# Kernel tuning notes

Hardware: AMD Instinct MI355X
Metric: run time of the kernel (lower is better)

The kernel has to match this reference:

```python
import jax, jax.numpy as jnp
import numpy as np

MEMORY_SLOTS = 256
MEMORY_TOPK = 8
RETRIEVAL_WEIGHT = 0.5


def setup_inputs() -> dict:
    key = jax.random.key(0)
    ks = jax.random.split(key, 5)
    B, T, C = 8, 2048, 1024
    scale = 1.0 / np.sqrt(C)
    return {
        "x": jax.random.normal(ks[0], (B, T, C), dtype=jnp.float32),
        "Wq": jax.random.normal(ks[1], (C, C), dtype=jnp.float32) * scale,
        "Wk": jax.random.normal(ks[2], (C, C), dtype=jnp.float32) * scale,
        "Wv": jax.random.normal(ks[3], (C, C), dtype=jnp.float32) * scale,
        "Wp": jax.random.normal(ks[4], (C, C), dtype=jnp.float32) * scale,
    }


def reference(x, Wq, Wk, Wv, Wp):
    B, T, C = x.shape
    num_slots = min(T, MEMORY_SLOTS)
    topk = min(num_slots, MEMORY_TOPK)
    # adaptive_avg_pool1d with T divisible by num_slots == mean over equal chunks
    slots = x.reshape(B, num_slots, T // num_slots, C).mean(axis=2)  # [B,S,C]
    # Linear layers (torch: x @ W.T, no bias)
    q = jnp.einsum("btc,dc->btd", x, Wq)        # [B,T,C]
    k = jnp.einsum("bsc,dc->bsd", slots, Wk)    # [B,S,C]
    v = jnp.einsum("bsc,dc->bsd", slots, Wv)    # [B,S,C]
    scores = jnp.einsum("btd,bsd->bts", q, k) * (1.0 / jnp.sqrt(jnp.float32(C)))
    topk_scores, topk_indices = jax.lax.top_k(scores, topk)  # [B,T,K]
    topk_weights = jax.nn.softmax(topk_scores, axis=-1)       # [B,T,K]
    # gather selected value rows: [B,T,K,C]
    retrieved = jnp.take_along_axis(v[:, None, :, :], topk_indices[..., None], axis=2)
    retrieved = jnp.einsum("btkc,btk->btc", retrieved, topk_weights)
    out = jnp.einsum("btc,dc->btd", retrieved, Wp) * RETRIEVAL_WEIGHT
    return out
```

## Files before the change

kernel.cpp:

```cpp
#include <hip/hip_runtime.h>
#include <cstdint>
#include <cstddef>

#define Tt 2048
#define Cc 1024
#define Ss 256

using short8 = __attribute__((ext_vector_type(8))) short;
using f32x4  = __attribute__((ext_vector_type(4))) float;
typedef const __attribute__((address_space(1))) void* as1_cvp;
typedef __attribute__((address_space(3))) void* as3_vp;

__device__ __forceinline__ unsigned short f2bf(float f) {
  unsigned int u = __float_as_uint(f);
  u += 0x7fffu + ((u >> 16) & 1u);
  return (unsigned short)(u >> 16);
}
__device__ __forceinline__ float bf2f(unsigned short h) {
  return __uint_as_float(((unsigned)h) << 16);
}
__device__ __forceinline__ void split3(float v, unsigned short& h, unsigned short& m, unsigned short& l) {
  h = f2bf(v);
  float r = v - bf2f(h);
  m = f2bf(r);
  l = f2bf(r - bf2f(m));
}

__device__ __forceinline__ int sw32(int row, int q) {
  return row * 32 + ((q ^ ((row >> 1) & 3)) << 3);
}

__global__ __launch_bounds__(256) void poolsplit_k(const float* __restrict__ x, unsigned short* __restrict__ sp) {
  const long PS2 = 2048l * 1024;
  const int sli = blockIdx.x;
  const int c = threadIdx.x << 2;
  const float* src = x + (size_t)sli * 8 * Cc + c;
  float a[4] = {0.f, 0.f, 0.f, 0.f};
#pragma unroll
  for (int j = 0; j < 8; j++) {
    float4 v = *(const float4*)(src + (size_t)j * Cc);
    a[0] += v.x; a[1] += v.y; a[2] += v.z; a[3] += v.w;
  }
  unsigned short h[4], m[4], l[4];
#pragma unroll
  for (int e = 0; e < 4; e++) split3(a[e] * 0.125f, h[e], m[e], l[e]);
  size_t o = (size_t)sli * Cc + c;
  *(uint2*)&sp[o]           = uint2{(unsigned)h[0] | ((unsigned)h[1] << 16), (unsigned)h[2] | ((unsigned)h[3] << 16)};
  *(uint2*)&sp[o + PS2]     = uint2{(unsigned)m[0] | ((unsigned)m[1] << 16), (unsigned)m[2] | ((unsigned)m[3] << 16)};
  *(uint2*)&sp[o + 2 * PS2] = uint2{(unsigned)l[0] | ((unsigned)l[1] << 16), (unsigned)l[2] | ((unsigned)l[3] << 16)};
}

__global__ __launch_bounds__(256) void split_t_k(const float* __restrict__ src, unsigned short* __restrict__ dst,
                                                 long pstride, int npl) {
  __shared__ unsigned short th[64][68], tm[64][68], tl[64][68];
  const int r0 = blockIdx.y << 6, c0 = blockIdx.x << 6;
  const int tid = threadIdx.x;
#pragma unroll
  for (int p = 0; p < 4; p++) {
    int r = (p << 4) + (tid >> 4);
    int c = (tid & 15) << 2;
    float4 v = *(const float4*)&src[(size_t)(r0 + r) * Cc + c0 + c];
    unsigned short h, m, l;
    split3(v.x, h, m, l); th[c + 0][r] = h; tm[c + 0][r] = m; tl[c + 0][r] = l;
    split3(v.y, h, m, l); th[c + 1][r] = h; tm[c + 1][r] = m; tl[c + 1][r] = l;
    split3(v.z, h, m, l); th[c + 2][r] = h; tm[c + 2][r] = m; tl[c + 2][r] = l;
    split3(v.w, h, m, l); th[c + 3][r] = h; tm[c + 3][r] = m; tl[c + 3][r] = l;
  }
  __syncthreads();
#pragma unroll
  for (int p = 0; p < 4; p++) {
    int r = (p << 4) + (tid >> 4);
    int c = (tid & 15) << 2;
    size_t o = (size_t)(c0 + r) * Cc + r0 + c;
    *(uint2*)&dst[o] = uint2{(unsigned)th[r][c] | ((unsigned)th[r][c+1] << 16),
                             (unsigned)th[r][c+2] | ((unsigned)th[r][c+3] << 16)};
    *(uint2*)&dst[o + pstride] = uint2{(unsigned)tm[r][c] | ((unsigned)tm[r][c+1] << 16),
                                       (unsigned)tm[r][c+2] | ((unsigned)tm[r][c+3] << 16)};
    if (npl == 3)
      *(uint2*)&dst[o + 2 * pstride] = uint2{(unsigned)tl[r][c] | ((unsigned)tl[r][c+1] << 16),
                                             (unsigned)tl[r][c+2] | ((unsigned)tl[r][c+3] << 16)};
  }
}

__global__ __launch_bounds__(256) void split_k(const float* __restrict__ src, unsigned short* __restrict__ dst,
                                               long pstride, int npl) {
  int id = blockIdx.x * 256 + threadIdx.x;
  int c = id << 2;
  float4 v = *(const float4*)&src[c];
  unsigned short h[4], m[4], l[4];
  split3(v.x, h[0], m[0], l[0]); split3(v.y, h[1], m[1], l[1]);
  split3(v.z, h[2], m[2], l[2]); split3(v.w, h[3], m[3], l[3]);
  *(uint2*)&dst[c] = uint2{(unsigned)h[0] | ((unsigned)h[1] << 16), (unsigned)h[2] | ((unsigned)h[3] << 16)};
  *(uint2*)&dst[c + pstride] = uint2{(unsigned)m[0] | ((unsigned)m[1] << 16), (unsigned)m[2] | ((unsigned)m[3] << 16)};
  if (npl == 3)
    *(uint2*)&dst[c + 2 * pstride] = uint2{(unsigned)l[0] | ((unsigned)l[1] << 16), (unsigned)l[2] | ((unsigned)l[3] << 16)};
}

template<int NT, int SPLIT_OUT>
__device__ __forceinline__ void gemm3_body(const unsigned short* __restrict__ Ap, long apl,
                                           const unsigned short* __restrict__ Bp, long bpl,
                                           float* __restrict__ C,
                                           unsigned short* __restrict__ Cs, long cpl,
                                           float scale) {
  constexpr int NPL = (NT == 6) ? 3 : 2;
  constexpr int BUFS = 2 * NPL * 2048;
  __shared__ unsigned short LDS[2 * BUFS];
  const int tid = threadIdx.x, lane = tid & 63, wid = tid >> 6;
  const int m0 = blockIdx.y << 6, n0 = blockIdx.x << 6;

  const unsigned short* sp[2 * NPL];
  int dof[2 * NPL];
#pragma unroll
  for (int i = 0; i < 2 * NPL; i++) {
    int s = wid * 2 * NPL + i;
    int tile = s >> 2;
    int ci = ((s & 3) << 6) | lane;
    int row = ci >> 2;
    int q = (ci & 3) ^ ((row >> 1) & 3);
    int isB = tile >= NPL;
    int pl = isB ? tile - NPL : tile;
    const unsigned short* base = isB ? (Bp + (size_t)pl * bpl) : (Ap + (size_t)pl * apl);
    int r0 = isB ? n0 : m0;
    sp[i] = base + (size_t)(r0 + row) * Cc + (q << 3);
    dof[i] = (tile * 2048 + ((s & 3) << 9)) * 2;
  }

  const int wm = (wid >> 1) << 5, wn = (wid & 1) << 5;
  const int lm = lane & 15, lq = lane >> 4;
  constexpr int PA[6] = {0, 0, 1, 0, 2, 1};
  constexpr int PB[6] = {0, 1, 0, 2, 0, 1};
  const f32x4 zero = {0.f, 0.f, 0.f, 0.f};
  f32x4 acc[2][2] = {{zero, zero}, {zero, zero}};

#pragma unroll
  for (int i = 0; i < 2 * NPL; i++) {
    __builtin_amdgcn_global_load_lds((as1_cvp)sp[i], (as3_vp)((char*)LDS + dof[i]), 16, 0, 0);
    sp[i] += 32;
  }
  __syncthreads();

  int cur = 0;
  for (int k0 = 0; k0 < Cc; k0 += 32) {
    if (k0 + 32 < Cc) {
      const int nb = (cur ^ 1) * (BUFS * 2);
#pragma unroll
      for (int i = 0; i < 2 * NPL; i++) {
        __builtin_amdgcn_global_load_lds((as1_cvp)sp[i], (as3_vp)((char*)LDS + nb + dof[i]), 16, 0, 0);
        sp[i] += 32;
      }
    }
    const int cb = cur * BUFS;
    short8 af[2][NPL], bf[2][NPL];
#pragma unroll
    for (int i = 0; i < 2; i++)
#pragma unroll
      for (int p = 0; p < NPL; p++) {
        af[i][p] = *(const short8*)&LDS[cb + p * 2048 + sw32(wm + (i << 4) + lm, lq)];
        bf[i][p] = *(const short8*)&LDS[cb + (NPL + p) * 2048 + sw32(wn + (i << 4) + lm, lq)];
      }
#pragma unroll
    for (int i = 0; i < 2; i++)
#pragma unroll
      for (int j = 0; j < 2; j++)
#pragma unroll
        for (int t = 0; t < NT; t++)
          acc[i][j] = __builtin_amdgcn_mfma_f32_16x16x32_bf16(af[i][PA[t]], bf[j][PB[t]], acc[i][j], 0, 0, 0);
    __syncthreads();
    cur ^= 1;
  }
#pragma unroll
  for (int i = 0; i < 2; i++)
#pragma unroll
    for (int j = 0; j < 2; j++)
#pragma unroll
      for (int r = 0; r < 4; r++) {
        int gr = m0 + wm + (i << 4) + (lq << 2) + r;
        int gc = n0 + wn + (j << 4) + lm;
        size_t o = (size_t)gr * Cc + gc;
        float v = acc[i][j][r] * scale;
        if (SPLIT_OUT) {
          unsigned short h = f2bf(v);
          float rr = v - bf2f(h);
          unsigned short mm2 = f2bf(rr);
          Cs[o] = h;
          Cs[o + cpl] = mm2;
          if (NPL == 3) Cs[o + 2 * (size_t)cpl] = f2bf(rr - bf2f(mm2));
        } else {
          C[o] = v;
        }
      }
}

__global__ __launch_bounds__(256) void gemm3_61_k(const unsigned short* __restrict__ Ap, long apl,
                                                  const unsigned short* __restrict__ Bp, long bpl,
                                                  unsigned short* __restrict__ Cs, long cpl, float scale) {
  gemm3_body<6, 1>(Ap, apl, Bp, bpl, nullptr, Cs, cpl, scale);
}
__global__ __launch_bounds__(256) void gemm3_31_k(const unsigned short* __restrict__ Ap, long apl,
                                                  const unsigned short* __restrict__ Bp, long bpl,
                                                  unsigned short* __restrict__ Cs, long cpl, float scale) {
  gemm3_body<3, 1>(Ap, apl, Bp, bpl, nullptr, Cs, cpl, scale);
}
__global__ __launch_bounds__(256) void gemm3_30_k(const unsigned short* __restrict__ Ap, long apl,
                                                  const unsigned short* __restrict__ Bp, long bpl,
                                                  float* __restrict__ C, float scale) {
  gemm3_body<3, 0>(Ap, apl, Bp, bpl, C, nullptr, 0, scale);
}

__global__ __launch_bounds__(512) void scores_topk_k(const float* __restrict__ x,
                                                     const unsigned short* __restrict__ kqp,
                                                     float* __restrict__ topw, int* __restrict__ topi) {
  __shared__ __align__(16) char smem[125952];
  unsigned short* lds16 = (unsigned short*)smem;
  float* sc = (float*)smem;

  const int tid = threadIdx.x, lane = tid & 63, wid = tid >> 6;
  const int bid = blockIdx.x;
  const int b = bid & 7, tt = bid >> 3;

  const char* ksrc[6];
  int kdst[6];
#pragma unroll
  for (int i = 0; i < 6; i++) {
    int s = wid * 6 + i;
    int p = s >> 4, sub = s & 15;
    int ci = (sub << 6) | lane;
    int row = ci >> 2;
    int q = (ci & 3) ^ ((row >> 1) & 3);
    ksrc[i] = (const char*)(kqp + (size_t)p * (2048l * 1024) + ((size_t)b * Ss + row) * Cc + (q << 3));
    kdst[i] = p * 16384 + sub * 1024;
  }
  const int spr = tid >> 3, spk = (tid & 7) << 2;
  const float* xsrc = x + ((size_t)b * Tt + (size_t)tt * 64 + spr) * Cc + spk;

  const int wm = (wid & 1) << 5;
  const int wn = (wid >> 1) << 6;
  const int lm = lane & 15, lq = lane >> 4;
  const int XP = 49152;

  constexpr int PA[6] = {0, 0, 1, 0, 2, 1};
  constexpr int PB[6] = {0, 1, 0, 2, 0, 1};
  const f32x4 zero = {0.f, 0.f, 0.f, 0.f};
  f32x4 acc[2][4];
#pragma unroll
  for (int i = 0; i < 2; i++)
#pragma unroll
    for (int j = 0; j < 4; j++) acc[i][j] = zero;

  {
    float4 xv = *(const float4*)xsrc; xsrc += 32;
#pragma unroll
    for (int i = 0; i < 6; i++) {
      __builtin_amdgcn_global_load_lds((as1_cvp)ksrc[i], (as3_vp)(smem + kdst[i]), 16, 0, 0);
      ksrc[i] += 64;
    }
    unsigned short h[4], m[4], l[4];
    split3(xv.x, h[0], m[0], l[0]); split3(xv.y, h[1], m[1], l[1]);
    split3(xv.z, h[2], m[2], l[2]); split3(xv.w, h[3], m[3], l[3]);
    int o = XP + spr * 36 + spk;
    *(uint2*)&lds16[o]        = uint2{(unsigned)h[0] | ((unsigned)h[1] << 16), (unsigned)h[2] | ((unsigned)h[3] << 16)};
    *(uint2*)&lds16[o + 2304] = uint2{(unsigned)m[0] | ((unsigned)m[1] << 16), (unsigned)m[2] | ((unsigned)m[3] << 16)};
    *(uint2*)&lds16[o + 4608] = uint2{(unsigned)l[0] | ((unsigned)l[1] << 16), (unsigned)l[2] | ((unsigned)l[3] << 16)};
  }
  __syncthreads();

  int cur = 0;
  for (int ks = 0; ks < 32; ks++) {
    const int nb = cur ^ 1;
    float4 xv2;
    if (ks < 31) {
      xv2 = *(const float4*)xsrc; xsrc += 32;
#pragma unroll
      for (int i = 0; i < 6; i++) {
        __builtin_amdgcn_global_load_lds((as1_cvp)ksrc[i], (as3_vp)(smem + nb * 49152 + kdst[i]), 16, 0, 0);
        ksrc[i] += 64;
      }
    }
    const int xb = XP + cur * 6912;
    const int kb = cur * 24576;
    short8 afr[2][3], bfr[4][3];
#pragma unroll
    for (int i = 0; i < 2; i++)
#pragma unroll
      for (int p = 0; p < 3; p++)
        afr[i][p] = *(const short8*)&lds16[xb + p * 2304 + (wm + (i << 4) + lm) * 36 + (lq << 3)];
#pragma unroll
    for (int j = 0; j < 4; j++) {
      int br = wn + (j << 4) + lm;
      int bo = (br << 5) + ((lq ^ ((br >> 1) & 3)) << 3);
#pragma unroll
      for (int p = 0; p < 3; p++)
        bfr[j][p] = *(const short8*)&lds16[kb + p * 8192 + bo];
    }
#pragma unroll
    for (int i = 0; i < 2; i++)
#pragma unroll
      for (int j = 0; j < 4; j++)
#pragma unroll
        for (int t = 0; t < 6; t++)
          acc[i][j] = __builtin_amdgcn_mfma_f32_16x16x32_bf16(afr[i][PA[t]], bfr[j][PB[t]], acc[i][j], 0, 0, 0);
    if (ks < 31) {
      unsigned short h[4], m[4], l[4];
      split3(xv2.x, h[0], m[0], l[0]); split3(xv2.y, h[1], m[1], l[1]);
      split3(xv2.z, h[2], m[2], l[2]); split3(xv2.w, h[3], m[3], l[3]);
      int o = XP + nb * 6912 + spr * 36 + spk;
      *(uint2*)&lds16[o]        = uint2{(unsigned)h[0] | ((unsigned)h[1] << 16), (unsigned)h[2] | ((unsigned)h[3] << 16)};
      *(uint2*)&lds16[o + 2304] = uint2{(unsigned)m[0] | ((unsigned)m[1] << 16), (unsigned)m[2] | ((unsigned)m[3] << 16)};
      *(uint2*)&lds16[o + 4608] = uint2{(unsigned)l[0] | ((unsigned)l[1] << 16), (unsigned)l[2] | ((unsigned)l[3] << 16)};
    }
    __syncthreads();
    cur ^= 1;
  }

#pragma unroll
  for (int i = 0; i < 2; i++)
#pragma unroll
    for (int j = 0; j < 4; j++)
#pragma unroll
      for (int r = 0; r < 4; r++)
        sc[(wm + (i << 4) + (lq << 2) + r) * 260 + wn + (j << 4) + lm] = acc[i][j][r] * 0.03125f;
  __syncthreads();

  for (int r2 = 0; r2 < 8; r2++) {
    int row = (wid << 3) + r2;
    float4 v = *(const float4*)(sc + row * 260 + (lane << 2));
    float cand[4] = {v.x, v.y, v.z, v.w};
    float topv[8]; int tops[8];
#pragma unroll
    for (int k = 0; k < 8; k++) {
      float bv = -1e30f; int bs = 1 << 20;
#pragma unroll
      for (int e = 0; e < 4; e++) {
        int s = (lane << 2) + e;
        if (cand[e] > bv || (cand[e] == bv && s < bs)) { bv = cand[e]; bs = s; }
      }
#pragma unroll
      for (int m = 32; m >= 1; m >>= 1) {
        float ov = __shfl_xor(bv, m, 64);
        int   os = __shfl_xor(bs, m, 64);
        if (ov > bv || (ov == bv && os < bs)) { bv = ov; bs = os; }
      }
      topv[k] = bv; tops[k] = bs;
      if ((bs >> 2) == lane) cand[bs & 3] = -1e30f;
    }
    float mx = topv[0];
    float sum = 0.f;
#pragma unroll
    for (int k = 0; k < 8; k++) sum += expf(topv[k] - mx);
    if (lane < 8) {
      float myv = topv[0]; int myi = tops[0];
#pragma unroll
      for (int k = 1; k < 8; k++) if (lane == k) { myv = topv[k]; myi = tops[k]; }
      size_t trow = (size_t)b * Tt + (size_t)tt * 64 + row;
      topw[trow * 8 + lane] = expf(myv - mx) / sum;
      topi[trow * 8 + lane] = myi;
    }
  }
}

__global__ __launch_bounds__(256) void gatherout_k(const float* __restrict__ u, const float* __restrict__ topw,
                                                   const int* __restrict__ topi, float* __restrict__ out) {
  __shared__ float w[8];
  __shared__ int  id8[8];
  const int row = blockIdx.x;
  const int b = row >> 11;
  if (threadIdx.x < 8) {
    w[threadIdx.x]   = topw[(size_t)row * 8 + threadIdx.x];
    id8[threadIdx.x] = topi[(size_t)row * 8 + threadIdx.x];
  }
  __syncthreads();
  int c = threadIdx.x << 2;
  float ax = 0.f, ay = 0.f, az = 0.f, aw = 0.f;
#pragma unroll
  for (int j = 0; j < 8; j++) {
    const float4 vv = *(const float4*)&u[((size_t)(b << 8) + id8[j]) * Cc + c];
    float wj = w[j];
    ax = fmaf(wj, vv.x, ax); ay = fmaf(wj, vv.y, ay);
    az = fmaf(wj, vv.z, az); aw = fmaf(wj, vv.w, aw);
  }
  *(float4*)&out[(size_t)row * Cc + c] = make_float4(ax * 0.5f, ay * 0.5f, az * 0.5f, aw * 0.5f);
}

extern "C" void kernel_launch(void* const* d_in, const int* in_sizes, int n_in,
                              void* d_out, int out_size, void* d_ws, size_t ws_size,
                              hipStream_t stream) {
  (void)in_sizes; (void)n_in; (void)out_size; (void)ws_size;
  const float* x  = (const float*)d_in[0];
  const float* Wq = (const float*)d_in[1];
  const float* Wk = (const float*)d_in[2];
  const float* Wv = (const float*)d_in[3];
  const float* Wp = (const float*)d_in[4];
  float* out = (float*)d_out;

  char* ws = (char*)d_ws;
  const size_t MB = 1ull << 20;
  const long PS1 = 1024l * 1024;
  const long PS2 = 2048l * 1024;
  unsigned short* slotp = (unsigned short*)(ws + 0 * MB);
  unsigned short* Wqt   = (unsigned short*)(ws + 12 * MB);
  unsigned short* Wkt   = (unsigned short*)(ws + 18 * MB);
  unsigned short* Wvt   = (unsigned short*)(ws + 24 * MB);
  unsigned short* Wpp   = (unsigned short*)(ws + 28 * MB);
  unsigned short* MtT   = (unsigned short*)(ws + 32 * MB);
  unsigned short* kqp   = (unsigned short*)(ws + 38 * MB);
  unsigned short* W2p   = (unsigned short*)(ws + 50 * MB);
  float*          u     = (float*)(ws + 54 * MB);
  float*          topw  = (float*)(ws + 62 * MB);
  int*            topi  = (int*)(ws + 62 * MB + 512 * 1024);

  poolsplit_k<<<2048, 256, 0, stream>>>(x, slotp);
  split_t_k<<<dim3(16, 16), 256, 0, stream>>>(Wq, Wqt, PS1, 3);
  split_t_k<<<dim3(16, 16), 256, 0, stream>>>(Wk, Wkt, PS1, 3);
  split_t_k<<<dim3(16, 16), 256, 0, stream>>>(Wv, Wvt, PS1, 2);
  split_k<<<1024, 256, 0, stream>>>(Wp, Wpp, PS1, 2);
  gemm3_61_k<<<dim3(16, 16), 256, 0, stream>>>(Wqt, PS1, Wkt, PS1, MtT, PS1, 1.0f);
  gemm3_61_k<<<dim3(16, 32), 256, 0, stream>>>(slotp, PS2, MtT, PS1, kqp, PS2, 1.0f);
  gemm3_31_k<<<dim3(16, 16), 256, 0, stream>>>(Wpp, PS1, Wvt, PS1, W2p, PS1, 1.0f);
  gemm3_30_k<<<dim3(16, 32), 256, 0, stream>>>(slotp, PS2, W2p, PS1, u, 1.0f);
  scores_topk_k<<<256, 512, 0, stream>>>(x, kqp, topw, topi);
  gatherout_k<<<16384, 256, 0, stream>>>(u, topw, topi, out);
}
```

Before: 380.2 us.

## Split scores/top-k over slot halves and merge partial top-8 lists

The scores+top-k kernel now handles only half of the 256 memory slots per block, which doubles the grid from 256 to 512 blocks and halves LDS use and accumulator registers. Each block writes a partial top-8 with global slot indices, and a new topmerge kernel merges the two halves and applies the softmax. The goal is better occupancy on a GPU with many CUs, since 256 blocks under-fill the device. The cost is that every block redoes the x-tile loading and 3-way bf16 splitting, plus an extra launch and a round trip of the partial lists through global memory.

New measurement: 418.6 us. +10.1%, slower.

```diff
diff --git a/kernel.cpp b/kernel.cpp
--- a/kernel.cpp
+++ b/kernel.cpp
@@ -207,57 +207,55 @@
   gemm3_body<3, 0>(Ap, apl, Bp, bpl, C, nullptr, 0, scale);
 }
 
-__global__ __launch_bounds__(512) void scores_topk_k(const float* __restrict__ x,
-                                                     const unsigned short* __restrict__ kqp,
-                                                     float* __restrict__ topw, int* __restrict__ topi) {
-  __shared__ __align__(16) char smem[125952];
+__global__ __launch_bounds__(512, 4) void scores_topk_k(const float* __restrict__ x,
+                                                        const unsigned short* __restrict__ kqp,
+                                                        float* __restrict__ hv, int* __restrict__ hi) {
+  __shared__ __align__(16) char smem[76800];
   unsigned short* lds16 = (unsigned short*)smem;
   float* sc = (float*)smem;
 
   const int tid = threadIdx.x, lane = tid & 63, wid = tid >> 6;
   const int bid = blockIdx.x;
-  const int b = bid & 7, tt = bid >> 3;
-
-  const char* ksrc[6];
-  int kdst[6];
-#pragma unroll
-  for (int i = 0; i < 6; i++) {
-    int s = wid * 6 + i;
-    int p = s >> 4, sub = s & 15;
+  const int b = bid & 7, half = (bid >> 3) & 1, tt = bid >> 4;
+  const int s0 = half << 7;
+
+  const char* ksrc[3];
+  int kdst[3];
+#pragma unroll
+  for (int i = 0; i < 3; i++) {
+    int s = wid * 3 + i;
+    int p = s >> 3, sub = s & 7;
     int ci = (sub << 6) | lane;
     int row = ci >> 2;
     int q = (ci & 3) ^ ((row >> 1) & 3);
-    ksrc[i] = (const char*)(kqp + (size_t)p * (2048l * 1024) + ((size_t)b * Ss + row) * Cc + (q << 3));
-    kdst[i] = p * 16384 + sub * 1024;
+    ksrc[i] = (const char*)(kqp + (size_t)p * (2048l * 1024) + ((size_t)b * Ss + s0 + row) * Cc + (q << 3));
+    kdst[i] = p * 8192 + sub * 1024;
   }
   const int spr = tid >> 3, spk = (tid & 7) << 2;
   const float* xsrc = x + ((size_t)b * Tt + (size_t)tt * 64 + spr) * Cc + spk;
 
   const int wm = (wid & 1) << 5;
-  const int wn = (wid >> 1) << 6;
+  const int wn = (wid >> 1) << 5;
   const int lm = lane & 15, lq = lane >> 4;
-  const int XP = 49152;
+  const int XPs = 24576;
+  const int KQB = 24576;
 
   constexpr int PA[6] = {0, 0, 1, 0, 2, 1};
   constexpr int PB[6] = {0, 1, 0, 2, 0, 1};
   const f32x4 zero = {0.f, 0.f, 0.f, 0.f};
-  f32x4 acc[2][4];
-#pragma unroll
-  for (int i = 0; i < 2; i++)
-#pragma unroll
-    for (int j = 0; j < 4; j++) acc[i][j] = zero;
+  f32x4 acc[2][2] = {{zero, zero}, {zero, zero}};
 
   {
     float4 xv = *(const float4*)xsrc; xsrc += 32;
 #pragma unroll
-    for (int i = 0; i < 6; i++) {
+    for (int i = 0; i < 3; i++) {
       __builtin_amdgcn_global_load_lds((as1_cvp)ksrc[i], (as3_vp)(smem + kdst[i]), 16, 0, 0);
       ksrc[i] += 64;
     }
     unsigned short h[4], m[4], l[4];
     split3(xv.x, h[0], m[0], l[0]); split3(xv.y, h[1], m[1], l[1]);
     split3(xv.z, h[2], m[2], l[2]); split3(xv.w, h[3], m[3], l[3]);
-    int o = XP + spr * 36 + spk;
+    int o = XPs + spr * 36 + spk;
     *(uint2*)&lds16[o]        = uint2{(unsigned)h[0] | ((unsigned)h[1] << 16), (unsigned)h[2] | ((unsigned)h[3] << 16)};
     *(uint2*)&lds16[o + 2304] = uint2{(unsigned)m[0] | ((unsigned)m[1] << 16), (unsigned)m[2] | ((unsigned)m[3] << 16)};
     *(uint2*)&lds16[o + 4608] = uint2{(unsigned)l[0] | ((unsigned)l[1] << 16), (unsigned)l[2] | ((unsigned)l[3] << 16)};
@@ -271,31 +269,31 @@
     if (ks < 31) {
       xv2 = *(const float4*)xsrc; xsrc += 32;
 #pragma unroll
-      for (int i = 0; i < 6; i++) {
-        __builtin_amdgcn_global_load_lds((as1_cvp)ksrc[i], (as3_vp)(smem + nb * 49152 + kdst[i]), 16, 0, 0);
+      for (int i = 0; i < 3; i++) {
+        __builtin_amdgcn_global_load_lds((as1_cvp)ksrc[i], (as3_vp)(smem + nb * KQB + kdst[i]), 16, 0, 0);
         ksrc[i] += 64;
       }
     }
-    const int xb = XP + cur * 6912;
-    const int kb = cur * 24576;
-    short8 afr[2][3], bfr[4][3];
+    const int xb = XPs + cur * 6912;
+    const int kb = cur * 12288;
+    short8 afr[2][3], bfr[2][3];
 #pragma unroll
     for (int i = 0; i < 2; i++)
 #pragma unroll
       for (int p = 0; p < 3; p++)
         afr[i][p] = *(const short8*)&lds16[xb + p * 2304 + (wm + (i << 4) + lm) * 36 + (lq << 3)];
 #pragma unroll
-    for (int j = 0; j < 4; j++) {
+    for (int j = 0; j < 2; j++) {
       int br = wn + (j << 4) + lm;
       int bo = (br << 5) + ((lq ^ ((br >> 1) & 3)) << 3);
 #pragma unroll
       for (int p = 0; p < 3; p++)
-        bfr[j][p] = *(const short8*)&lds16[kb + p * 8192 + bo];
+        bfr[j][p] = *(const short8*)&lds16[kb + p * 4096 + bo];
     }
 #pragma unroll
     for (int i = 0; i < 2; i++)
 #pragma unroll
-      for (int j = 0; j < 4; j++)
+      for (int j = 0; j < 2; j++)
 #pragma unroll
         for (int t = 0; t < 6; t++)
           acc[i][j] = __builtin_amdgcn_mfma_f32_16x16x32_bf16(afr[i][PA[t]], bfr[j][PB[t]], acc[i][j], 0, 0, 0);
@@ -303,7 +301,7 @@
       unsigned short h[4], m[4], l[4];
       split3(xv2.x, h[0], m[0], l[0]); split3(xv2.y, h[1], m[1], l[1]);
       split3(xv2.z, h[2], m[2], l[2]); split3(xv2.w, h[3], m[3], l[3]);
-      int o = XP + nb * 6912 + spr * 36 + spk;
+      int o = XPs + nb * 6912 + spr * 36 + spk;
       *(uint2*)&lds16[o]        = uint2{(unsigned)h[0] | ((unsigned)h[1] << 16), (unsigned)h[2] | ((unsigned)h[3] << 16)};
       *(uint2*)&lds16[o + 2304] = uint2{(unsigned)m[0] | ((unsigned)m[1] << 16), (unsigned)m[2] | ((unsigned)m[3] << 16)};
       *(uint2*)&lds16[o + 4608] = uint2{(unsigned)l[0] | ((unsigned)l[1] << 16), (unsigned)l[2] | ((unsigned)l[3] << 16)};
@@ -315,23 +313,23 @@
 #pragma unroll
   for (int i = 0; i < 2; i++)
 #pragma unroll
-    for (int j = 0; j < 4; j++)
+    for (int j = 0; j < 2; j++)
 #pragma unroll
       for (int r = 0; r < 4; r++)
-        sc[(wm + (i << 4) + (lq << 2) + r) * 260 + wn + (j << 4) + lm] = acc[i][j][r] * 0.03125f;
+        sc[(wm + (i << 4) + (lq << 2) + r) * 132 + wn + (j << 4) + lm] = acc[i][j][r] * 0.03125f;
   __syncthreads();
 
   for (int r2 = 0; r2 < 8; r2++) {
     int row = (wid << 3) + r2;
-    float4 v = *(const float4*)(sc + row * 260 + (lane << 2));
-    float cand[4] = {v.x, v.y, v.z, v.w};
+    float2 v2 = *(const float2*)(sc + row * 132 + (lane << 1));
+    float cand[2] = {v2.x, v2.y};
     float topv[8]; int tops[8];
 #pragma unroll
     for (int k = 0; k < 8; k++) {
       float bv = -1e30f; int bs = 1 << 20;
 #pragma unroll
-      for (int e = 0; e < 4; e++) {
-        int s = (lane << 2) + e;
+      for (int e = 0; e < 2; e++) {
+        int s = (lane << 1) + e;
         if (cand[e] > bv || (cand[e] == bv && s < bs)) { bv = cand[e]; bs = s; }
       }
 #pragma unroll
@@ -341,20 +339,51 @@
         if (ov > bv || (ov == bv && os < bs)) { bv = ov; bs = os; }
       }
       topv[k] = bv; tops[k] = bs;
-      if ((bs >> 2) == lane) cand[bs & 3] = -1e30f;
-    }
-    float mx = topv[0];
-    float sum = 0.f;
-#pragma unroll
-    for (int k = 0; k < 8; k++) sum += expf(topv[k] - mx);
+      if ((bs >> 1) == lane) cand[bs & 1] = -1e30f;
+    }
     if (lane < 8) {
       float myv = topv[0]; int myi = tops[0];
 #pragma unroll
       for (int k = 1; k < 8; k++) if (lane == k) { myv = topv[k]; myi = tops[k]; }
       size_t trow = (size_t)b * Tt + (size_t)tt * 64 + row;
-      topw[trow * 8 + lane] = expf(myv - mx) / sum;
-      topi[trow * 8 + lane] = myi;
-    }
+      hv[trow * 16 + (half << 3) + lane] = myv;
+      hi[trow * 16 + (half << 3) + lane] = s0 + myi;
+    }
+  }
+}
+
+__global__ __launch_bounds__(256) void topmerge_k(const float* __restrict__ hv, const int* __restrict__ hi,
+                                                  float* __restrict__ topw, int* __restrict__ topi) {
+  const int row = blockIdx.x * 256 + threadIdx.x;
+  float v[16]; int ix[16];
+#pragma unroll
+  for (int g = 0; g < 4; g++) {
+    float4 a = *(const float4*)(hv + (size_t)row * 16 + (g << 2));
+    int4  c = *(const int4*)(hi + (size_t)row * 16 + (g << 2));
+    v[(g << 2) + 0] = a.x; v[(g << 2) + 1] = a.y; v[(g << 2) + 2] = a.z; v[(g << 2) + 3] = a.w;
+    ix[(g << 2) + 0] = c.x; ix[(g << 2) + 1] = c.y; ix[(g << 2) + 2] = c.z; ix[(g << 2) + 3] = c.w;
+  }
+  float ov[8]; int oi[8];
+#pragma unroll
+  for (int k = 0; k < 8; k++) {
+    float bv = -1e30f; int bi = 1 << 30;
+#pragma unroll
+    for (int e = 0; e < 16; e++)
+      if (v[e] > bv || (v[e] == bv && ix[e] < bi)) { bv = v[e]; bi = ix[e]; }
+    ov[k] = bv; oi[k] = bi;
+#pragma unroll
+    for (int e = 0; e < 16; e++)
+      if (v[e] == bv && ix[e] == bi) v[e] = -1e30f;
+  }
+  const float mx = ov[0];
+  float w[8]; float sum = 0.f;
+#pragma unroll
+  for (int k = 0; k < 8; k++) { w[k] = expf(ov[k] - mx); sum += w[k]; }
+  const float inv = 1.f / sum;
+#pragma unroll
+  for (int k = 0; k < 8; k++) {
+    topw[(size_t)row * 8 + k] = w[k] * inv;
+    topi[(size_t)row * 8 + k] = oi[k];
   }
 }
 
@@ -407,6 +436,8 @@
   float*          u     = (float*)(ws + 54 * MB);
   float*          topw  = (float*)(ws + 62 * MB);
   int*            topi  = (int*)(ws + 62 * MB + 512 * 1024);
+  float*          hv    = (float*)(ws + 63 * MB);
+  int*            hi    = (int*)(ws + 64 * MB);
 
   poolsplit_k<<<2048, 256, 0, stream>>>(x, slotp);
   split_t_k<<<dim3(16, 16), 256, 0, stream>>>(Wq, Wqt, PS1, 3);
@@ -417,6 +448,7 @@
   gemm3_61_k<<<dim3(16, 32), 256, 0, stream>>>(slotp, PS2, MtT, PS1, kqp, PS2, 1.0f);
   gemm3_31_k<<<dim3(16, 16), 256, 0, stream>>>(Wpp, PS1, Wvt, PS1, W2p, PS1, 1.0f);
   gemm3_30_k<<<dim3(16, 32), 256, 0, stream>>>(slotp, PS2, W2p, PS1, u, 1.0f);
-  scores_topk_k<<<256, 512, 0, stream>>>(x, kqp, topw, topi);
+  scores_topk_k<<<512, 512, 0, stream>>>(x, kqp, hv, hi);
+  topmerge_k<<<64, 256, 0, stream>>>(hv, hi, topw, topi);
   gatherout_k<<<16384, 256, 0, stream>>>(u, topw, topi, out);
 }
```

## Load K fragments directly from global into registers, shrink LDS for two blocks/CU

Applied to the files above, without the earlier changes.

The scores/top-k kernel no longer stages the three-way-split K matrix through double-buffered LDS with global_load_lds. Each wave now reads its B fragments straight from global memory into registers every k-step. Only the x tile stays in LDS. This cuts the shared memory footprint enough to request two 512-thread blocks per CU, aiming for higher occupancy. The trade-off is that the global load latency of K is no longer prefetched, so it sits directly in front of the MFMAs, and there is redundant global traffic across waves that share columns.

New measurement: 404.6 us. +6.4%, slower.

```diff
diff --git a/kernel.cpp b/kernel.cpp
--- a/kernel.cpp
+++ b/kernel.cpp
@@ -207,10 +207,10 @@
   gemm3_body<3, 0>(Ap, apl, Bp, bpl, C, nullptr, 0, scale);
 }
 
-__global__ __launch_bounds__(512) void scores_topk_k(const float* __restrict__ x,
-                                                     const unsigned short* __restrict__ kqp,
-                                                     float* __restrict__ topw, int* __restrict__ topi) {
-  __shared__ __align__(16) char smem[125952];
+__global__ __launch_bounds__(512, 2) void scores_topk_k(const float* __restrict__ x,
+                                                        const unsigned short* __restrict__ kqp,
+                                                        float* __restrict__ topw, int* __restrict__ topi) {
+  __shared__ __align__(16) char smem[66560];
   unsigned short* lds16 = (unsigned short*)smem;
   float* sc = (float*)smem;
 
@@ -218,25 +218,15 @@
   const int bid = blockIdx.x;
   const int b = bid & 7, tt = bid >> 3;
 
-  const char* ksrc[6];
-  int kdst[6];
-#pragma unroll
-  for (int i = 0; i < 6; i++) {
-    int s = wid * 6 + i;
-    int p = s >> 4, sub = s & 15;
-    int ci = (sub << 6) | lane;
-    int row = ci >> 2;
-    int q = (ci & 3) ^ ((row >> 1) & 3);
-    ksrc[i] = (const char*)(kqp + (size_t)p * (2048l * 1024) + ((size_t)b * Ss + row) * Cc + (q << 3));
-    kdst[i] = p * 16384 + sub * 1024;
-  }
   const int spr = tid >> 3, spk = (tid & 7) << 2;
   const float* xsrc = x + ((size_t)b * Tt + (size_t)tt * 64 + spr) * Cc + spk;
 
   const int wm = (wid & 1) << 5;
   const int wn = (wid >> 1) << 6;
   const int lm = lane & 15, lq = lane >> 4;
-  const int XP = 49152;
+
+  const long KPL = 2048l * 1024;
+  const unsigned short* kqb = kqp + ((size_t)b * Ss + wn + lm) * Cc + (lq << 3);
 
   constexpr int PA[6] = {0, 0, 1, 0, 2, 1};
   constexpr int PB[6] = {0, 1, 0, 2, 0, 1};
@@ -249,15 +239,10 @@
 
   {
     float4 xv = *(const float4*)xsrc; xsrc += 32;
-#pragma unroll
-    for (int i = 0; i < 6; i++) {
-      __builtin_amdgcn_global_load_lds((as1_cvp)ksrc[i], (as3_vp)(smem + kdst[i]), 16, 0, 0);
-      ksrc[i] += 64;
-    }
     unsigned short h[4], m[4], l[4];
     split3(xv.x, h[0], m[0], l[0]); split3(xv.y, h[1], m[1], l[1]);
     split3(xv.z, h[2], m[2], l[2]); split3(xv.w, h[3], m[3], l[3]);
-    int o = XP + spr * 36 + spk;
+    int o = spr * 36 + spk;
     *(uint2*)&lds16[o]        = uint2{(unsigned)h[0] | ((unsigned)h[1] << 16), (unsigned)h[2] | ((unsigned)h[3] << 16)};
     *(uint2*)&lds16[o + 2304] = uint2{(unsigned)m[0] | ((unsigned)m[1] << 16), (unsigned)m[2] | ((unsigned)m[3] << 16)};
     *(uint2*)&lds16[o + 4608] = uint2{(unsigned)l[0] | ((unsigned)l[1] << 16), (unsigned)l[2] | ((unsigned)l[3] << 16)};
@@ -267,31 +252,22 @@
   int cur = 0;
   for (int ks = 0; ks < 32; ks++) {
     const int nb = cur ^ 1;
+    const int k0 = ks << 5;
     float4 xv2;
-    if (ks < 31) {
-      xv2 = *(const float4*)xsrc; xsrc += 32;
-#pragma unroll
-      for (int i = 0; i < 6; i++) {
-        __builtin_amdgcn_global_load_lds((as1_cvp)ksrc[i], (as3_vp)(smem + nb * 49152 + kdst[i]), 16, 0, 0);
-        ksrc[i] += 64;
-      }
-    }
-    const int xb = XP + cur * 6912;
-    const int kb = cur * 24576;
-    short8 afr[2][3], bfr[4][3];
+    if (ks < 31) { xv2 = *(const float4*)xsrc; xsrc += 32; }
+    short8 bfr[4][3];
+#pragma unroll
+    for (int j = 0; j < 4; j++)
+#pragma unroll
+      for (int p = 0; p < 3; p++)
+        bfr[j][p] = *(const short8*)(kqb + (size_t)p * KPL + (size_t)(j << 4) * Cc + k0);
+    const int xb = cur * 6912;
+    short8 afr[2][3];
 #pragma unroll
     for (int i = 0; i < 2; i++)
 #pragma unroll
       for (int p = 0; p < 3; p++)
         afr[i][p] = *(const short8*)&lds16[xb + p * 2304 + (wm + (i << 4) + lm) * 36 + (lq << 3)];
-#pragma unroll
-    for (int j = 0; j < 4; j++) {
-      int br = wn + (j << 4) + lm;
-      int bo = (br << 5) + ((lq ^ ((br >> 1) & 3)) << 3);
-#pragma unroll
-      for (int p = 0; p < 3; p++)
-        bfr[j][p] = *(const short8*)&lds16[kb + p * 8192 + bo];
-    }
 #pragma unroll
     for (int i = 0; i < 2; i++)
 #pragma unroll
@@ -303,7 +279,7 @@
       unsigned short h[4], m[4], l[4];
       split3(xv2.x, h[0], m[0], l[0]); split3(xv2.y, h[1], m[1], l[1]);
       split3(xv2.z, h[2], m[2], l[2]); split3(xv2.w, h[3], m[3], l[3]);
-      int o = XP + nb * 6912 + spr * 36 + spk;
+      int o = nb * 6912 + spr * 36 + spk;
       *(uint2*)&lds16[o]        = uint2{(unsigned)h[0] | ((unsigned)h[1] << 16), (unsigned)h[2] | ((unsigned)h[3] << 16)};
       *(uint2*)&lds16[o + 2304] = uint2{(unsigned)m[0] | ((unsigned)m[1] << 16), (unsigned)m[2] | ((unsigned)m[3] << 16)};
       *(uint2*)&lds16[o + 4608] = uint2{(unsigned)l[0] | ((unsigned)l[1] << 16), (unsigned)l[2] | ((unsigned)l[3] << 16)};
```

## Batch independent GEMMs into shared launches and use 128x128 tiles for slot GEMMs

Applied to the files above, without the earlier changes.

Merges the two independent weight-product GEMMs into a single launch that picks its branch from blockIdx.z. It does the same for the two slot GEMMs, and those now use a new 128x128-tile body with 4x4 MFMA accumulators per wave. The aim is to cut launch count, fill more CUs per launch, and raise data reuse per LDS tile in the larger GEMMs. The cost is more LDS (96KB) and more registers per block, which may lower occupancy. The z=0 and z=1 branches also do unequal amounts of work, so the load is imbalanced.

After: 361.9 us. 4.8% less time.

```diff
diff --git a/kernel.cpp b/kernel.cpp
--- a/kernel.cpp
+++ b/kernel.cpp
@@ -97,14 +97,14 @@
 }
 
 template<int NT, int SPLIT_OUT>
-__device__ __forceinline__ void gemm3_body(const unsigned short* __restrict__ Ap, long apl,
+__device__ __forceinline__ void gemm3_body(unsigned short* LDS,
+                                           const unsigned short* __restrict__ Ap, long apl,
                                            const unsigned short* __restrict__ Bp, long bpl,
                                            float* __restrict__ C,
                                            unsigned short* __restrict__ Cs, long cpl,
                                            float scale) {
   constexpr int NPL = (NT == 6) ? 3 : 2;
   constexpr int BUFS = 2 * NPL * 2048;
-  __shared__ unsigned short LDS[2 * BUFS];
   const int tid = threadIdx.x, lane = tid & 63, wid = tid >> 6;
   const int m0 = blockIdx.y << 6, n0 = blockIdx.x << 6;
 
@@ -191,20 +191,131 @@
       }
 }
 
-__global__ __launch_bounds__(256) void gemm3_61_k(const unsigned short* __restrict__ Ap, long apl,
-                                                  const unsigned short* __restrict__ Bp, long bpl,
-                                                  unsigned short* __restrict__ Cs, long cpl, float scale) {
-  gemm3_body<6, 1>(Ap, apl, Bp, bpl, nullptr, Cs, cpl, scale);
-}
-__global__ __launch_bounds__(256) void gemm3_31_k(const unsigned short* __restrict__ Ap, long apl,
-                                                  const unsigned short* __restrict__ Bp, long bpl,
-                                                  unsigned short* __restrict__ Cs, long cpl, float scale) {
-  gemm3_body<3, 1>(Ap, apl, Bp, bpl, nullptr, Cs, cpl, scale);
-}
-__global__ __launch_bounds__(256) void gemm3_30_k(const unsigned short* __restrict__ Ap, long apl,
-                                                  const unsigned short* __restrict__ Bp, long bpl,
-                                                  float* __restrict__ C, float scale) {
-  gemm3_body<3, 0>(Ap, apl, Bp, bpl, C, nullptr, 0, scale);
+template<int NT, int SPLIT_OUT>
+__device__ __forceinline__ void gemm128_body(unsigned short* LDS,
+                                             const unsigned short* __restrict__ Ap, long apl,
+                                             const unsigned short* __restrict__ Bp, long bpl,
+                                             float* __restrict__ C,
+                                             unsigned short* __restrict__ Cs, long cpl,
+                                             float scale) {
+  constexpr int NPL = (NT == 6) ? 3 : 2;
+  constexpr int BUFS = 2 * NPL * 4096;
+  const int tid = threadIdx.x, lane = tid & 63, wid = tid >> 6;
+  const int m0 = blockIdx.y << 7, n0 = blockIdx.x << 7;
+
+  const unsigned short* sp[4 * NPL];
+  int dof[4 * NPL];
+#pragma unroll
+  for (int i = 0; i < 4 * NPL; i++) {
+    int s = wid * 4 * NPL + i;
+    int tile = s >> 3;
+    int ci = ((s & 7) << 6) | lane;
+    int row = ci >> 2;
+    int q = (ci & 3) ^ ((row >> 1) & 3);
+    int isB = tile >= NPL;
+    int pl = isB ? tile - NPL : tile;
+    const unsigned short* base = isB ? (Bp + (size_t)pl * bpl) : (Ap + (size_t)pl * apl);
+    int r0 = isB ? n0 : m0;
+    sp[i] = base + (size_t)(r0 + row) * Cc + (q << 3);
+    dof[i] = (tile * 4096 + ((s & 7) << 9)) * 2;
+  }
+
+  const int wr = (wid >> 1) << 6, wc = (wid & 1) << 6;
+  const int lm = lane & 15, lq = lane >> 4;
+  constexpr int PA[6] = {0, 0, 1, 0, 2, 1};
+  constexpr int PB[6] = {0, 1, 0, 2, 0, 1};
+  const f32x4 zero = {0.f, 0.f, 0.f, 0.f};
+  f32x4 acc[4][4];
+#pragma unroll
+  for (int i = 0; i < 4; i++)
+#pragma unroll
+    for (int j = 0; j < 4; j++) acc[i][j] = zero;
+
+#pragma unroll
+  for (int i = 0; i < 4 * NPL; i++) {
+    __builtin_amdgcn_global_load_lds((as1_cvp)sp[i], (as3_vp)((char*)LDS + dof[i]), 16, 0, 0);
+    sp[i] += 32;
+  }
+  __syncthreads();
+
+  int cur = 0;
+  for (int k0 = 0; k0 < Cc; k0 += 32) {
+    if (k0 + 32 < Cc) {
+      const int nb = (cur ^ 1) * (BUFS * 2);
+#pragma unroll
+      for (int i = 0; i < 4 * NPL; i++) {
+        __builtin_amdgcn_global_load_lds((as1_cvp)sp[i], (as3_vp)((char*)LDS + nb + dof[i]), 16, 0, 0);
+        sp[i] += 32;
+      }
+    }
+    const int cb = cur * BUFS;
+    short8 af[4][NPL];
+#pragma unroll
+    for (int i = 0; i < 4; i++)
+#pragma unroll
+      for (int p = 0; p < NPL; p++)
+        af[i][p] = *(const short8*)&LDS[cb + p * 4096 + sw32(wr + (i << 4) + lm, lq)];
+#pragma unroll
+    for (int j = 0; j < 4; j++) {
+      short8 bf[NPL];
+#pragma unroll
+      for (int p = 0; p < NPL; p++)
+        bf[p] = *(const short8*)&LDS[cb + (NPL + p) * 4096 + sw32(wc + (j << 4) + lm, lq)];
+#pragma unroll
+      for (int i = 0; i < 4; i++)
+#pragma unroll
+        for (int t = 0; t < NT; t++)
+          acc[i][j] = __builtin_amdgcn_mfma_f32_16x16x32_bf16(af[i][PA[t]], bf[PB[t]], acc[i][j], 0, 0, 0);
+    }
+    __syncthreads();
+    cur ^= 1;
+  }
+#pragma unroll
+  for (int i = 0; i < 4; i++)
+#pragma unroll
+    for (int j = 0; j < 4; j++)
+#pragma unroll
+      for (int r = 0; r < 4; r++) {
+        int gr = m0 + wr + (i << 4) + (lq << 2) + r;
+        int gc = n0 + wc + (j << 4) + lm;
+        size_t o = (size_t)gr * Cc + gc;
+        float v = acc[i][j][r] * scale;
+        if (SPLIT_OUT) {
+          unsigned short h = f2bf(v);
+          float rr = v - bf2f(h);
+          unsigned short mm2 = f2bf(rr);
+          Cs[o] = h;
+          Cs[o + cpl] = mm2;
+          if (NPL == 3) Cs[o + 2 * (size_t)cpl] = f2bf(rr - bf2f(mm2));
+        } else {
+          C[o] = v;
+        }
+      }
+}
+
+__global__ __launch_bounds__(256) void gemm35_k(const unsigned short* __restrict__ Wqt,
+                                                const unsigned short* __restrict__ Wkt,
+                                                const unsigned short* __restrict__ Wpp,
+                                                const unsigned short* __restrict__ Wvt,
+                                                unsigned short* __restrict__ MtT,
+                                                unsigned short* __restrict__ W2p, long ps1) {
+  __shared__ unsigned short LDS[24576];
+  if (blockIdx.z == 0)
+    gemm3_body<6, 1>(LDS, Wqt, ps1, Wkt, ps1, nullptr, MtT, ps1, 1.0f);
+  else
+    gemm3_body<3, 1>(LDS, Wpp, ps1, Wvt, ps1, nullptr, W2p, ps1, 1.0f);
+}
+
+__global__ __launch_bounds__(256) void gemm46_k(const unsigned short* __restrict__ slotp, long ps2,
+                                                const unsigned short* __restrict__ MtT,
+                                                const unsigned short* __restrict__ W2p, long ps1,
+                                                unsigned short* __restrict__ kqp,
+                                                float* __restrict__ u) {
+  __shared__ unsigned short LDS[49152];
+  if (blockIdx.z == 0)
+    gemm128_body<6, 1>(LDS, slotp, ps2, MtT, ps1, nullptr, kqp, ps2, 1.0f);
+  else
+    gemm128_body<3, 0>(LDS, slotp, ps2, W2p, ps1, u, nullptr, 0, 1.0f);
 }
 
 __global__ __launch_bounds__(512) void scores_topk_k(const float* __restrict__ x,
@@ -413,10 +524,8 @@
   split_t_k<<<dim3(16, 16), 256, 0, stream>>>(Wk, Wkt, PS1, 3);
   split_t_k<<<dim3(16, 16), 256, 0, stream>>>(Wv, Wvt, PS1, 2);
   split_k<<<1024, 256, 0, stream>>>(Wp, Wpp, PS1, 2);
-  gemm3_61_k<<<dim3(16, 16), 256, 0, stream>>>(Wqt, PS1, Wkt, PS1, MtT, PS1, 1.0f);
-  gemm3_61_k<<<dim3(16, 32), 256, 0, stream>>>(slotp, PS2, MtT, PS1, kqp, PS2, 1.0f);
-  gemm3_31_k<<<dim3(16, 16), 256, 0, stream>>>(Wpp, PS1, Wvt, PS1, W2p, PS1, 1.0f);
-  gemm3_30_k<<<dim3(16, 32), 256, 0, stream>>>(slotp, PS2, W2p, PS1, u, 1.0f);
+  gemm35_k<<<dim3(16, 16, 2), 256, 0, stream>>>(Wqt, Wkt, Wpp, Wvt, MtT, W2p, PS1);
+  gemm46_k<<<dim3(8, 16, 2), 256, 0, stream>>>(slotp, PS2, MtT, W2p, PS1, kqp, u);
   scores_topk_k<<<256, 512, 0, stream>>>(x, kqp, topw, topi);
   gatherout_k<<<16384, 256, 0, stream>>>(u, topw, topi, out);
 }
```
